# Performance work log

Hardware: AMD Instinct MI355X
Metric: run time of the kernel (lower is better)

## Reference

```python
import jax, jax.numpy as jnp
import numpy as np

N = 50000       # nodes
E = 800000      # edges (before self-loops)
F_IN = 128      # num_features
HID = 32        # hidden_dim per head
HEADS = 8
C = 40          # num_classes
NEG_SLOPE = 0.2 # PyG GATConv default leaky_relu slope


def setup_inputs() -> dict:
    key = jax.random.key(0)
    ks = jax.random.split(key, 10)
    x = jax.random.normal(ks[0], (N, F_IN), jnp.float32)
    edge_index = jax.random.randint(ks[1], (2, E), 0, N, dtype=jnp.int64)
    W1 = jax.random.normal(ks[2], (F_IN, HEADS * HID), jnp.float32) * np.float32(1.0 / np.sqrt(F_IN))
    a1_src = jax.random.normal(ks[3], (HEADS, HID), jnp.float32) * 0.1
    a1_dst = jax.random.normal(ks[4], (HEADS, HID), jnp.float32) * 0.1
    b1 = jnp.zeros((HEADS * HID,), jnp.float32)
    W2 = jax.random.normal(ks[5], (HEADS * HID, C), jnp.float32) * np.float32(1.0 / np.sqrt(HEADS * HID))
    a2_src = jax.random.normal(ks[6], (1, C), jnp.float32) * 0.1
    a2_dst = jax.random.normal(ks[7], (1, C), jnp.float32) * 0.1
    b2 = jnp.zeros((C,), jnp.float32)
    return {"x": x, "edge_index": edge_index,
            "W1": W1, "a1_src": a1_src, "a1_dst": a1_dst, "b1": b1,
            "W2": W2, "a2_src": a2_src, "a2_dst": a2_dst, "b2": b2}


def gat_conv(x, edge_index, W, a_src, a_dst, bias):
    """PyG-style GATConv (concat heads, add_self_loops=True), inference mode (no dropout)."""
    n = x.shape[0]
    heads, out_dim = a_src.shape
    ar = jnp.arange(n, dtype=edge_index.dtype)
    src = jnp.concatenate([edge_index[0], ar])   # [E+N]
    dst = jnp.concatenate([edge_index[1], ar])   # [E+N]
    h = (x @ W).reshape(n, heads, out_dim)       # [N, H, D]
    alpha_src = jnp.einsum('nhd,hd->nh', h, a_src)  # [N, H]
    alpha_dst = jnp.einsum('nhd,hd->nh', h, a_dst)  # [N, H]
    e = jax.nn.leaky_relu(alpha_src[src] + alpha_dst[dst], NEG_SLOPE)  # [E+N, H]
    # segment softmax over edges grouped by destination node
    m = jax.ops.segment_max(e, dst, num_segments=n)          # [N, H]
    ex = jnp.exp(e - m[dst])                                  # [E+N, H]
    s = jax.ops.segment_sum(ex, dst, num_segments=n)          # [N, H]
    alpha = ex / (s[dst] + 1e-16)                              # [E+N, H]
    msg = h[src] * alpha[..., None]                            # [E+N, H, D]
    out = jax.ops.segment_sum(msg, dst, num_segments=n)       # [N, H, D]
    return out.reshape(n, heads * out_dim) + bias


def reference(x, edge_index, W1, a1_src, a1_dst, b1, W2, a2_src, a2_dst, b2):
    h = jax.nn.elu(gat_conv(x, edge_index, W1, a1_src, a1_dst, b1))
    # F.dropout is identity in eval mode
    return gat_conv(h, edge_index, W2, a2_src, a2_dst, b2)
```

## Files before the change

### kernel.cpp

```cpp
#include <hip/hip_runtime.h>
#include <math.h>

#define F_IN 128
#define HID 32
#define HEADS 8
#define HD 256
#define NC 40
#define NCP 48
#define H2S 64
#define CAP 96
#define NEG 0.2f

typedef _Float16 half8 __attribute__((ext_vector_type(8)));
typedef float f32x4 __attribute__((ext_vector_type(4)));

__device__ __forceinline__ float leaky(float v) { return v > 0.0f ? v : NEG * v; }
__device__ __forceinline__ float2 up2(unsigned int u) {
    union { unsigned int u; _Float16 h[2]; } c; c.u = u;
    return make_float2((float)c.h[0], (float)c.h[1]);
}

__global__ __launch_bounds__(256) void prep_scatter_k(const int* __restrict__ ei,
        int* __restrict__ cnt, int* __restrict__ esrc,
        const float* __restrict__ W1, const float* __restrict__ W2,
        const float* __restrict__ a1s, const float* __restrict__ a1d,
        const float* __restrict__ a2s, const float* __restrict__ a2d,
        _Float16* __restrict__ W1t, _Float16* __restrict__ W2t,
        _Float16* __restrict__ Pt, int E) {
    int i = blockIdx.x * 256 + threadIdx.x;
    if (i < E) {
        int src = ei[i], dst = ei[E + i];
        int pos = atomicAdd(&cnt[dst], 1);
        esrc[dst * CAP + pos] = src;
        return;
    }
    int w1i = i - E;
    if (w1i < HD * F_IN) {
        int c = w1i >> 7, k = w1i & 127;
        W1t[w1i] = (_Float16)W1[k * HD + c];
        return;
    }
    int w2i = w1i - HD * F_IN;
    if (w2i < NCP * HD) {
        int c = w2i >> 8, k = w2i & 255;
        float v = 0.0f;
        if (c < NC) {
            v = W2[k * NC + c];
        } else if (c == NC || c == NC + 1) {
            const float* av = (c == NC) ? a2s : a2d;
            for (int d = 0; d < NC; ++d) v = fmaf(W2[k * NC + d], av[d], v);
        }
        W2t[w2i] = (_Float16)v;
        return;
    }
    int p = w2i - NCP * HD;
    if (p < 16 * F_IN) {
        int pj = p >> 7, k = p & 127;
        int h = pj & 7;
        const float* av = (pj < 8) ? (a1s + h * HID) : (a1d + h * HID);
        const float* wr = W1 + (size_t)k * HD + h * HID;
        float acc = 0.0f;
#pragma unroll 8
        for (int d = 0; d < HID; ++d) acc = fmaf(wr[d], av[d], acc);
        Pt[pj * F_IN + k] = (_Float16)acc;
    }
}

__global__ __launch_bounds__(256) void gemm1_k(const float* __restrict__ x,
        const _Float16* __restrict__ W1t, const _Float16* __restrict__ Pt,
        _Float16* __restrict__ H1, float* __restrict__ asrc,
        float* __restrict__ adst, int N) {
    int t = threadIdx.x;
    int w = t >> 6, l = t & 63;
    int quad = l >> 4, lr = l & 15;
    int rowA = blockIdx.x * 64 + w * 16 + lr;
    int rowL = rowA < N ? rowA : N - 1;

    half8 af[4];
    const float* xr = x + (size_t)rowL * F_IN + quad * 8;
#pragma unroll
    for (int s = 0; s < 4; ++s) {
        float4 u = *(const float4*)(xr + s * 32);
        float4 v = *(const float4*)(xr + s * 32 + 4);
        half8 a;
        a[0] = (_Float16)u.x; a[1] = (_Float16)u.y;
        a[2] = (_Float16)u.z; a[3] = (_Float16)u.w;
        a[4] = (_Float16)v.x; a[5] = (_Float16)v.y;
        a[6] = (_Float16)v.z; a[7] = (_Float16)v.w;
        af[s] = a;
    }

    int rowC0 = blockIdx.x * 64 + w * 16 + quad * 4;
#pragma unroll
    for (int tt = 0; tt < 16; ++tt) {
        f32x4 acc = {0.0f, 0.0f, 0.0f, 0.0f};
        const _Float16* wp = W1t + (size_t)(tt * 16 + lr) * F_IN + quad * 8;
#pragma unroll
        for (int s = 0; s < 4; ++s) {
            half8 b = *(const half8*)(wp + s * 32);
            acc = __builtin_amdgcn_mfma_f32_16x16x32_f16(af[s], b, acc, 0, 0, 0);
        }
#pragma unroll
        for (int r = 0; r < 4; ++r) {
            int rr = rowC0 + r;
            if (rr < N) H1[(size_t)rr * HD + tt * 16 + lr] = (_Float16)acc[r];
        }
    }
    {
        f32x4 acc = {0.0f, 0.0f, 0.0f, 0.0f};
        const _Float16* pp = Pt + (size_t)lr * F_IN + quad * 8;
#pragma unroll
        for (int s = 0; s < 4; ++s) {
            half8 b = *(const half8*)(pp + s * 32);
            acc = __builtin_amdgcn_mfma_f32_16x16x32_f16(af[s], b, acc, 0, 0, 0);
        }
#pragma unroll
        for (int r = 0; r < 4; ++r) {
            int rr = rowC0 + r;
            if (rr < N) {
                if (lr < 8) asrc[rr * HEADS + lr] = acc[r];
                else        adst[rr * HEADS + (lr - 8)] = acc[r];
            }
        }
    }
}

__global__ __launch_bounds__(256) void agg1g2_k(const int* __restrict__ esrc,
        const int* __restrict__ cnt, const float* __restrict__ asrc,
        const float* __restrict__ adst, const _Float16* __restrict__ H1,
        const float* __restrict__ b1, const _Float16* __restrict__ W2t,
        _Float16* __restrict__ H2h, float* __restrict__ asrc2,
        float* __restrict__ adst2, int N) {
    __shared__ _Float16 rows[16][HD];
    int t = threadIdx.x;
    int c = t & 31;
    int ld = t >> 5;
    int dst = blockIdx.x * 8 + ld;
    int dstc = dst < N ? dst : N - 1;
    int h = c >> 2;
    int start = dstc * CAP;
    int end = start + cnt[dstc];
    float adh = adst[dstc * HEADS + h];

    float ws = __expf(leaky(asrc[dstc * HEADS + h] + adh));
    float s = ws;
    float acc[8];
    {
        uint4 hs = *(const uint4*)(H1 + (size_t)dstc * HD + c * 8);
        float2 p0 = up2(hs.x), p1 = up2(hs.y), p2 = up2(hs.z), p3 = up2(hs.w);
        acc[0] = p0.x * ws; acc[1] = p0.y * ws;
        acc[2] = p1.x * ws; acc[3] = p1.y * ws;
        acc[4] = p2.x * ws; acc[5] = p2.y * ws;
        acc[6] = p3.x * ws; acc[7] = p3.y * ws;
    }

    int e = start;
    for (; e + 3 < end; e += 4) {
        int si[4]; float al[4]; uint4 hv[4];
#pragma unroll
        for (int q = 0; q < 4; ++q) si[q] = esrc[e + q];
#pragma unroll
        for (int q = 0; q < 4; ++q) {
            al[q] = asrc[si[q] * HEADS + h];
            hv[q] = *(const uint4*)(H1 + (size_t)si[q] * HD + c * 8);
        }
#pragma unroll
        for (int q = 0; q < 4; ++q) {
            float w = __expf(leaky(al[q] + adh));
            s += w;
            float2 p0 = up2(hv[q].x), p1 = up2(hv[q].y);
            float2 p2 = up2(hv[q].z), p3 = up2(hv[q].w);
            acc[0] = fmaf(p0.x, w, acc[0]); acc[1] = fmaf(p0.y, w, acc[1]);
            acc[2] = fmaf(p1.x, w, acc[2]); acc[3] = fmaf(p1.y, w, acc[3]);
            acc[4] = fmaf(p2.x, w, acc[4]); acc[5] = fmaf(p2.y, w, acc[5]);
            acc[6] = fmaf(p3.x, w, acc[6]); acc[7] = fmaf(p3.y, w, acc[7]);
        }
    }
    for (; e < end; ++e) {
        int s0 = esrc[e];
        float al0 = asrc[s0 * HEADS + h];
        uint4 h0 = *(const uint4*)(H1 + (size_t)s0 * HD + c * 8);
        float w0 = __expf(leaky(al0 + adh));
        s += w0;
        float2 p0 = up2(h0.x), p1 = up2(h0.y);
        float2 p2 = up2(h0.z), p3 = up2(h0.w);
        acc[0] = fmaf(p0.x, w0, acc[0]); acc[1] = fmaf(p0.y, w0, acc[1]);
        acc[2] = fmaf(p1.x, w0, acc[2]); acc[3] = fmaf(p1.y, w0, acc[3]);
        acc[4] = fmaf(p2.x, w0, acc[4]); acc[5] = fmaf(p2.y, w0, acc[5]);
        acc[6] = fmaf(p3.x, w0, acc[6]); acc[7] = fmaf(p3.y, w0, acc[7]);
    }
    float inv = 1.0f / (s + 1e-16f);
    float4 b0 = *(const float4*)(b1 + c * 8);
    float4 b4 = *(const float4*)(b1 + c * 8 + 4);
    float o[8];
    o[0] = fmaf(acc[0], inv, b0.x); o[1] = fmaf(acc[1], inv, b0.y);
    o[2] = fmaf(acc[2], inv, b0.z); o[3] = fmaf(acc[3], inv, b0.w);
    o[4] = fmaf(acc[4], inv, b4.x); o[5] = fmaf(acc[5], inv, b4.y);
    o[6] = fmaf(acc[6], inv, b4.z); o[7] = fmaf(acc[7], inv, b4.w);
    half8 ov, zv;
#pragma unroll
    for (int q = 0; q < 8; ++q) {
        float v = o[q] > 0.0f ? o[q] : expm1f(o[q]);
        ov[q] = (_Float16)v;
        zv[q] = (_Float16)0.0f;
    }
    *(half8*)&rows[ld][c * 8] = ov;
    *(half8*)&rows[8 + ld][c * 8] = zv;
    __syncthreads();

    if (t < 64) {
        int quad = t >> 4, lr = t & 15;
        half8 af[8];
#pragma unroll
        for (int sfs = 0; sfs < 8; ++sfs)
            af[sfs] = *(const half8*)&rows[lr][sfs * 32 + quad * 8];
        f32x4 ga[3];
#pragma unroll
        for (int tt = 0; tt < 3; ++tt) {
            f32x4 a = {0.0f, 0.0f, 0.0f, 0.0f};
            const _Float16* wp = W2t + (size_t)(tt * 16 + lr) * HD + quad * 8;
#pragma unroll
            for (int sfs = 0; sfs < 8; ++sfs) {
                half8 b = *(const half8*)(wp + sfs * 32);
                a = __builtin_amdgcn_mfma_f32_16x16x32_f16(af[sfs], b, a, 0, 0, 0);
            }
            ga[tt] = a;
        }
        int row0 = quad * 4;
#pragma unroll
        for (int tt = 0; tt < 3; ++tt) {
            int c2 = tt * 16 + lr;
#pragma unroll
            for (int r = 0; r < 4; ++r) {
                int row = row0 + r;
                if (row < 8) {
                    int g = blockIdx.x * 8 + row;
                    if (g < N) {
                        float v = ga[tt][r];
                        if (c2 < NC)            H2h[(size_t)g * H2S + c2] = (_Float16)v;
                        else if (c2 == NC)      asrc2[g] = v;
                        else if (c2 == NC + 1)  adst2[g] = v;
                    }
                }
            }
        }
    }
}

__global__ __launch_bounds__(256) void agg2_k(const int* __restrict__ esrc,
        const int* __restrict__ cnt, const float* __restrict__ asrc,
        const float* __restrict__ adst, const _Float16* __restrict__ H2h,
        const float* __restrict__ b2, float* __restrict__ dout, int N) {
    int t = threadIdx.x;
    int c = t & 31;
    int dst = blockIdx.x * 8 + (t >> 5);
    if (dst >= N) return;
    int start = dst * CAP;
    int end = start + cnt[dst];
    float adst_v = adst[dst];

    float ws = __expf(leaky(asrc[dst] + adst_v));
    float s = ws;
    float a0, a1;
    {
        unsigned int hv = *(const unsigned int*)(H2h + (size_t)dst * H2S + c * 2);
        float2 p = up2(hv);
        a0 = p.x * ws; a1 = p.y * ws;
    }

    int e = start;
    for (; e + 7 < end; e += 8) {
        int si[8]; float al[8]; unsigned int v[8];
#pragma unroll
        for (int q = 0; q < 8; ++q) si[q] = esrc[e + q];
#pragma unroll
        for (int q = 0; q < 8; ++q) {
            al[q] = asrc[si[q]];
            v[q] = *(const unsigned int*)(H2h + (size_t)si[q] * H2S + c * 2);
        }
#pragma unroll
        for (int q = 0; q < 8; ++q) {
            float w = __expf(leaky(al[q] + adst_v));
            s += w;
            float2 p = up2(v[q]);
            a0 = fmaf(p.x, w, a0);
            a1 = fmaf(p.y, w, a1);
        }
    }
    for (; e + 3 < end; e += 4) {
        int si[4]; float al[4]; unsigned int v[4];
#pragma unroll
        for (int q = 0; q < 4; ++q) si[q] = esrc[e + q];
#pragma unroll
        for (int q = 0; q < 4; ++q) {
            al[q] = asrc[si[q]];
            v[q] = *(const unsigned int*)(H2h + (size_t)si[q] * H2S + c * 2);
        }
#pragma unroll
        for (int q = 0; q < 4; ++q) {
            float w = __expf(leaky(al[q] + adst_v));
            s += w;
            float2 p = up2(v[q]);
            a0 = fmaf(p.x, w, a0);
            a1 = fmaf(p.y, w, a1);
        }
    }
    for (; e < end; ++e) {
        int s0 = esrc[e];
        float w0 = __expf(leaky(asrc[s0] + adst_v));
        s += w0;
        float2 p = up2(*(const unsigned int*)(H2h + (size_t)s0 * H2S + c * 2));
        a0 = fmaf(p.x, w0, a0);
        a1 = fmaf(p.y, w0, a1);
    }
    if (c * 2 < NC) {
        float inv = 1.0f / (s + 1e-16f);
        float2 o;
        o.x = fmaf(a0, inv, b2[c * 2]);
        o.y = fmaf(a1, inv, b2[c * 2 + 1]);
        *(float2*)(dout + (size_t)dst * NC + c * 2) = o;
    }
}

extern "C" void kernel_launch(void* const* d_in, const int* in_sizes, int n_in,
                              void* d_out, int out_size, void* d_ws, size_t ws_size,
                              hipStream_t stream) {
    const float* x   = (const float*)d_in[0];
    const int*   ei  = (const int*)d_in[1];
    const float* W1  = (const float*)d_in[2];
    const float* a1s = (const float*)d_in[3];
    const float* a1d = (const float*)d_in[4];
    const float* b1  = (const float*)d_in[5];
    const float* W2  = (const float*)d_in[6];
    const float* a2s = (const float*)d_in[7];
    const float* a2d = (const float*)d_in[8];
    const float* b2  = (const float*)d_in[9];
    float* dout = (float*)d_out;

    int N = in_sizes[0] / F_IN;
    int E = in_sizes[1] / 2;

    char* base = (char*)d_ws;
    size_t off = 0;
    auto carve = [&](size_t bytes) { char* p = base + off; off += (bytes + 255) & ~(size_t)255; return p; };
    _Float16* H1   = (_Float16*)carve((size_t)N * HD * 2);
    _Float16* W1t  = (_Float16*)carve((size_t)HD * F_IN * 2);
    _Float16* W2t  = (_Float16*)carve((size_t)NCP * HD * 2);
    _Float16* Pt   = (_Float16*)carve((size_t)16 * F_IN * 2);
    _Float16* H2h  = (_Float16*)carve((size_t)N * H2S * 2);
    float* asrc1  = (float*)carve((size_t)N * HEADS * 4);
    float* adst1  = (float*)carve((size_t)N * HEADS * 4);
    float* asrc2  = (float*)carve((size_t)N * 4);
    float* adst2  = (float*)carve((size_t)N * 4);
    int*   cnt    = (int*)carve((size_t)N * 4);
    int*   esrc   = (int*)carve((size_t)N * CAP * 4);

    hipMemsetAsync(cnt, 0, (size_t)N * 4, stream);
    int prep_total = E + HD * F_IN + NCP * HD + 16 * F_IN;
    hipLaunchKernelGGL(prep_scatter_k, dim3((prep_total + 255) / 256), dim3(256), 0, stream,
                       ei, cnt, esrc, W1, W2, a1s, a1d, a2s, a2d, W1t, W2t, Pt, E);

    hipLaunchKernelGGL(gemm1_k, dim3((N + 63) / 64), dim3(256), 0, stream,
                       x, W1t, Pt, H1, asrc1, adst1, N);
    hipLaunchKernelGGL(agg1g2_k, dim3((N + 7) / 8), dim3(256), 0, stream,
                       esrc, cnt, asrc1, adst1, H1, b1, W2t, H2h, asrc2, adst2, N);
    hipLaunchKernelGGL(agg2_k, dim3((N + 7) / 8), dim3(256), 0, stream,
                       esrc, cnt, asrc2, adst2, H2h, b2, dout, N);
}
```

Baseline: 267.8 us.

## Sort neighbor lists, vectorize GEMM1 stores, unroll aggregation by 8, split GEMM2 across waves

Adds a per-node insertion sort of the bucketed source indices so neighbor gathers run in ascending address order, which may improve cache locality. GEMM1 swaps its MFMA operands so each lane writes contiguous packed half4 and float4 outputs instead of scattered scalar stores. Layer-1 aggregation gains an 8-way unrolled gather loop, a launch-bounds occupancy hint, and padded shared rows. The GEMM2 tail is split across three waves instead of one. The extra sort kernel adds a serial per-thread pass with divergent loop lengths.

```diff
diff --git a/kernel.cpp b/kernel.cpp
--- a/kernel.cpp
+++ b/kernel.cpp
@@ -10,8 +10,10 @@
 #define H2S 64
 #define CAP 96
 #define NEG 0.2f
+#define RPAD 8
 
 typedef _Float16 half8 __attribute__((ext_vector_type(8)));
+typedef _Float16 half4v __attribute__((ext_vector_type(4)));
 typedef float f32x4 __attribute__((ext_vector_type(4)));
 
 __device__ __forceinline__ float leaky(float v) { return v > 0.0f ? v : NEG * v; }
@@ -66,6 +68,20 @@
     }
 }
 
+__global__ __launch_bounds__(256) void sort_k(const int* __restrict__ cnt,
+        int* __restrict__ esrc, int N) {
+    int d = blockIdx.x * 256 + threadIdx.x;
+    if (d >= N) return;
+    int n = cnt[d];
+    int* b = esrc + d * CAP;
+    for (int i = 1; i < n; ++i) {
+        int v = b[i];
+        int j = i - 1;
+        while (j >= 0 && b[j] > v) { b[j + 1] = b[j]; --j; }
+        b[j + 1] = v;
+    }
+}
+
 __global__ __launch_bounds__(256) void gemm1_k(const float* __restrict__ x,
         const _Float16* __restrict__ W1t, const _Float16* __restrict__ Pt,
         _Float16* __restrict__ H1, float* __restrict__ asrc,
@@ -75,6 +91,7 @@
     int quad = l >> 4, lr = l & 15;
     int rowA = blockIdx.x * 64 + w * 16 + lr;
     int rowL = rowA < N ? rowA : N - 1;
+    bool ok = rowA < N;
 
     half8 af[4];
     const float* xr = x + (size_t)rowL * F_IN + quad * 8;
@@ -90,7 +107,6 @@
         af[s] = a;
     }
 
-    int rowC0 = blockIdx.x * 64 + w * 16 + quad * 4;
 #pragma unroll
     for (int tt = 0; tt < 16; ++tt) {
         f32x4 acc = {0.0f, 0.0f, 0.0f, 0.0f};
@@ -98,12 +114,13 @@
 #pragma unroll
         for (int s = 0; s < 4; ++s) {
             half8 b = *(const half8*)(wp + s * 32);
-            acc = __builtin_amdgcn_mfma_f32_16x16x32_f16(af[s], b, acc, 0, 0, 0);
-        }
-#pragma unroll
-        for (int r = 0; r < 4; ++r) {
-            int rr = rowC0 + r;
-            if (rr < N) H1[(size_t)rr * HD + tt * 16 + lr] = (_Float16)acc[r];
+            acc = __builtin_amdgcn_mfma_f32_16x16x32_f16(b, af[s], acc, 0, 0, 0);
+        }
+        if (ok) {
+            half4v pk;
+            pk[0] = (_Float16)acc[0]; pk[1] = (_Float16)acc[1];
+            pk[2] = (_Float16)acc[2]; pk[3] = (_Float16)acc[3];
+            *(half4v*)(H1 + (size_t)rowA * HD + tt * 16 + quad * 4) = pk;
         }
     }
     {
@@ -112,26 +129,23 @@
 #pragma unroll
         for (int s = 0; s < 4; ++s) {
             half8 b = *(const half8*)(pp + s * 32);
-            acc = __builtin_amdgcn_mfma_f32_16x16x32_f16(af[s], b, acc, 0, 0, 0);
-        }
-#pragma unroll
-        for (int r = 0; r < 4; ++r) {
-            int rr = rowC0 + r;
-            if (rr < N) {
-                if (lr < 8) asrc[rr * HEADS + lr] = acc[r];
-                else        adst[rr * HEADS + (lr - 8)] = acc[r];
-            }
-        }
-    }
-}
-
-__global__ __launch_bounds__(256) void agg1g2_k(const int* __restrict__ esrc,
+            acc = __builtin_amdgcn_mfma_f32_16x16x32_f16(b, af[s], acc, 0, 0, 0);
+        }
+        if (ok) {
+            float4 v4 = make_float4(acc[0], acc[1], acc[2], acc[3]);
+            if (quad < 2) *(float4*)(asrc + (size_t)rowA * HEADS + quad * 4) = v4;
+            else          *(float4*)(adst + (size_t)rowA * HEADS + (quad - 2) * 4) = v4;
+        }
+    }
+}
+
+__global__ __launch_bounds__(256, 4) void agg1g2_k(const int* __restrict__ esrc,
         const int* __restrict__ cnt, const float* __restrict__ asrc,
         const float* __restrict__ adst, const _Float16* __restrict__ H1,
         const float* __restrict__ b1, const _Float16* __restrict__ W2t,
         _Float16* __restrict__ H2h, float* __restrict__ asrc2,
         float* __restrict__ adst2, int N) {
-    __shared__ _Float16 rows[16][HD];
+    __shared__ _Float16 rows[16][HD + RPAD];
     int t = threadIdx.x;
     int c = t & 31;
     int ld = t >> 5;
@@ -155,6 +169,27 @@
     }
 
     int e = start;
+    for (; e + 7 < end; e += 8) {
+        int si[8]; float al[8]; uint4 hv[8];
+#pragma unroll
+        for (int q = 0; q < 8; ++q) si[q] = esrc[e + q];
+#pragma unroll
+        for (int q = 0; q < 8; ++q) {
+            al[q] = asrc[si[q] * HEADS + h];
+            hv[q] = *(const uint4*)(H1 + (size_t)si[q] * HD + c * 8);
+        }
+#pragma unroll
+        for (int q = 0; q < 8; ++q) {
+            float w = __expf(leaky(al[q] + adh));
+            s += w;
+            float2 p0 = up2(hv[q].x), p1 = up2(hv[q].y);
+            float2 p2 = up2(hv[q].z), p3 = up2(hv[q].w);
+            acc[0] = fmaf(p0.x, w, acc[0]); acc[1] = fmaf(p0.y, w, acc[1]);
+            acc[2] = fmaf(p1.x, w, acc[2]); acc[3] = fmaf(p1.y, w, acc[3]);
+            acc[4] = fmaf(p2.x, w, acc[4]); acc[5] = fmaf(p2.y, w, acc[5]);
+            acc[6] = fmaf(p3.x, w, acc[6]); acc[7] = fmaf(p3.y, w, acc[7]);
+        }
+    }
     for (; e + 3 < end; e += 4) {
         int si[4]; float al[4]; uint4 hv[4];
 #pragma unroll
@@ -208,39 +243,33 @@
     *(half8*)&rows[8 + ld][c * 8] = zv;
     __syncthreads();
 
-    if (t < 64) {
-        int quad = t >> 4, lr = t & 15;
-        half8 af[8];
+    int wv = t >> 6;
+    if (wv < 3) {
+        int lt = t & 63;
+        int quad = lt >> 4, lr = lt & 15;
+        half8 af2[8];
 #pragma unroll
         for (int sfs = 0; sfs < 8; ++sfs)
-            af[sfs] = *(const half8*)&rows[lr][sfs * 32 + quad * 8];
-        f32x4 ga[3];
-#pragma unroll
-        for (int tt = 0; tt < 3; ++tt) {
-            f32x4 a = {0.0f, 0.0f, 0.0f, 0.0f};
-            const _Float16* wp = W2t + (size_t)(tt * 16 + lr) * HD + quad * 8;
-#pragma unroll
-            for (int sfs = 0; sfs < 8; ++sfs) {
-                half8 b = *(const half8*)(wp + sfs * 32);
-                a = __builtin_amdgcn_mfma_f32_16x16x32_f16(af[sfs], b, a, 0, 0, 0);
-            }
-            ga[tt] = a;
+            af2[sfs] = *(const half8*)&rows[lr][sfs * 32 + quad * 8];
+        f32x4 a = {0.0f, 0.0f, 0.0f, 0.0f};
+        const _Float16* wp = W2t + (size_t)(wv * 16 + lr) * HD + quad * 8;
+#pragma unroll
+        for (int sfs = 0; sfs < 8; ++sfs) {
+            half8 b = *(const half8*)(wp + sfs * 32);
+            a = __builtin_amdgcn_mfma_f32_16x16x32_f16(af2[sfs], b, a, 0, 0, 0);
         }
         int row0 = quad * 4;
-#pragma unroll
-        for (int tt = 0; tt < 3; ++tt) {
-            int c2 = tt * 16 + lr;
-#pragma unroll
-            for (int r = 0; r < 4; ++r) {
-                int row = row0 + r;
-                if (row < 8) {
-                    int g = blockIdx.x * 8 + row;
-                    if (g < N) {
-                        float v = ga[tt][r];
-                        if (c2 < NC)            H2h[(size_t)g * H2S + c2] = (_Float16)v;
-                        else if (c2 == NC)      asrc2[g] = v;
-                        else if (c2 == NC + 1)  adst2[g] = v;
-                    }
+        int c2 = wv * 16 + lr;
+#pragma unroll
+        for (int r = 0; r < 4; ++r) {
+            int row = row0 + r;
+            if (row < 8) {
+                int g = blockIdx.x * 8 + row;
+                if (g < N) {
+                    float v = a[r];
+                    if (c2 < NC)            H2h[(size_t)g * H2S + c2] = (_Float16)v;
+                    else if (c2 == NC)      asrc2[g] = v;
+                    else if (c2 == NC + 1)  adst2[g] = v;
                 }
             }
         }
@@ -359,6 +388,8 @@
     int prep_total = E + HD * F_IN + NCP * HD + 16 * F_IN;
     hipLaunchKernelGGL(prep_scatter_k, dim3((prep_total + 255) / 256), dim3(256), 0, stream,
                        ei, cnt, esrc, W1, W2, a1s, a1d, a2s, a2d, W1t, W2t, Pt, E);
+    hipLaunchKernelGGL(sort_k, dim3((N + 255) / 256), dim3(256), 0, stream,
+                       cnt, esrc, N);
 
     hipLaunchKernelGGL(gemm1_k, dim3((N + 63) / 64), dim3(256), 0, stream,
                        x, W1t, Pt, H1, asrc1, adst1, N);
```

Result: slower. 373.8 us (+39.6%).
